# Kernel optimization log

Hardware: AMD Instinct MI355X
Metric: run time of the kernel (lower is better)

The kernel has to match this reference:

```python
import jax, jax.numpy as jnp
import numpy as np

B, S, D = 4, 2048, 1024
H = 16
HD = D // H  # 64


def setup_inputs() -> dict:
    key = jax.random.key(0)
    ks = jax.random.split(key, 8)
    scale = 1.0 / np.sqrt(D)
    return {
        "hidden_states": jax.random.normal(ks[0], (B, S, D), dtype=jnp.float32),
        "attention_mask": jnp.ones((B, 1, 1, S), dtype=jnp.int32),
        "Wq": jax.random.normal(ks[1], (D, D), dtype=jnp.float32) * scale,
        "bq": jax.random.normal(ks[2], (D,), dtype=jnp.float32) * 0.02,
        "Wk": jax.random.normal(ks[3], (D, D), dtype=jnp.float32) * scale,
        "bk": jax.random.normal(ks[4], (D,), dtype=jnp.float32) * 0.02,
        "Wv": jax.random.normal(ks[5], (D, D), dtype=jnp.float32) * scale,
        "bv": jax.random.normal(ks[6], (D,), dtype=jnp.float32) * 0.02,
    }


def _split_heads(x):
    # [b, t, (h d)] -> [b, h, t, d]
    b, t, _ = x.shape
    return x.reshape(b, t, H, HD).transpose(0, 2, 1, 3)


def reference(hidden_states, attention_mask, Wq, bq, Wk, bk, Wv, bv):
    # Linear projections (torch Linear: x @ W.T + b)
    q = _split_heads(hidden_states @ Wq.T + bq)
    k = _split_heads(hidden_states @ Wk.T + bk)
    v = _split_heads(hidden_states @ Wv.T + bv)

    # scaled dot-product scores: [b, h, s, s]
    scores = jnp.einsum("bhqd,bhkd->bhqk", q, k) / np.sqrt(HD)

    s = scores.shape[-1]
    causal = jnp.tril(jnp.ones((s, s), dtype=bool))[None, None]
    neg_inf = jnp.float32(-jnp.inf)
    scores = jnp.where(causal, scores, neg_inf)
    # attention_mask is 0/1 keep mask: [b, 1, 1, s]
    scores = jnp.where(attention_mask == 0, neg_inf, scores)

    probs = jax.nn.softmax(scores, axis=-1)  # dropout p=0 (eval)
    ctx = jnp.einsum("bhqk,bhkd->bhqd", probs, v)
    # [b, h, t, d] -> [b, t, h*d]
    return ctx.transpose(0, 2, 1, 3).reshape(hidden_states.shape[0], s, D)
```

## Files before the change

kernel.cpp:

```cpp
#include <hip/hip_runtime.h>
#include <hip/hip_bf16.h>
#include <math.h>


#define B_ 4
#define S_ 2048
#define D_ 1024
#define H_ 16
#define HD_ 64
#define M_ (B_ * S_)

typedef unsigned short u16;
typedef unsigned int u32;
typedef __attribute__((ext_vector_type(4))) float f32x4;
typedef __attribute__((ext_vector_type(8))) short bf16x8;

__device__ __forceinline__ u16 f2bfu_rn(float x) {
    u32 u = __builtin_bit_cast(u32, x);
    return (u16)((u + 0x8000u) >> 16);
}

__device__ __forceinline__ void gl2lds16(const void* g, void* l) {
    __builtin_amdgcn_global_load_lds(
        (const __attribute__((address_space(1))) u32*)g,
        (__attribute__((address_space(3))) u32*)l, 16, 0, 0);
}

#define XN  8388608u
#define WN  1048576u
__global__ __launch_bounds__(256) void convert_bf16(
    const float* __restrict__ X,  const float* __restrict__ Wq,
    const float* __restrict__ Wk, const float* __restrict__ Wv,
    u16* __restrict__ Xb, u16* __restrict__ Wqb,
    u16* __restrict__ Wkb, u16* __restrict__ Wvb)
{
    size_t idx = ((size_t)blockIdx.x * 256 + threadIdx.x) * 8;
    const float* src; u16* dst; size_t off;
    if (idx < XN)                { src = X;  dst = Xb;  off = idx; }
    else if (idx < XN + WN)      { src = Wq; dst = Wqb; off = idx - XN; }
    else if (idx < XN + 2 * WN)  { src = Wk; dst = Wkb; off = idx - XN - WN; }
    else                         { src = Wv; dst = Wvb; off = idx - XN - 2 * WN; }
    float4 a = *(const float4*)(src + off);
    float4 b = *(const float4*)(src + off + 4);
    uint4 o;
    o.x = (u32)f2bfu_rn(a.x) | ((u32)f2bfu_rn(a.y) << 16);
    o.y = (u32)f2bfu_rn(a.z) | ((u32)f2bfu_rn(a.w) << 16);
    o.z = (u32)f2bfu_rn(b.x) | ((u32)f2bfu_rn(b.y) << 16);
    o.w = (u32)f2bfu_rn(b.z) | ((u32)f2bfu_rn(b.w) << 16);
    *(uint4*)(dst + off) = o;
}

#define QSCALE 0.18033688011112042f

__global__ __launch_bounds__(256) void qkv_mfma(
    const u16* __restrict__ Xb,
    const u16* __restrict__ Wqb, const u16* __restrict__ Wkb,
    const u16* __restrict__ Wvb,
    const float* __restrict__ bq, const float* __restrict__ bk,
    const float* __restrict__ bv,
    u16* __restrict__ Qb, u16* __restrict__ Kb, u16* __restrict__ Vtb)
{
    const int which = blockIdx.z;
    const u16* Asrc; const u16* Bsrc; const float* bias; u16* Out;
    int m0, n0;
    if (which == 0)      { Asrc = Xb;  Bsrc = Wqb; bias = bq; Out = Qb;
                           m0 = blockIdx.y * 128; n0 = blockIdx.x * 128; }
    else if (which == 1) { Asrc = Xb;  Bsrc = Wkb; bias = bk; Out = Kb;
                           m0 = blockIdx.y * 128; n0 = blockIdx.x * 128; }
    else                 { Asrc = Wvb; Bsrc = Xb;  bias = bv; Out = Vtb;
                           m0 = blockIdx.x * 128; n0 = blockIdx.y * 128; }

    __shared__ u16 As[128][64];
    __shared__ u16 Bs[128][64];

    const int t = threadIdx.x;
    const int wave = t >> 6, lane = t & 63;
    const int qd = lane >> 4, l15 = lane & 15;
    const int wm = wave >> 1, wn = wave & 1;

    const f32x4 zero = {0.f, 0.f, 0.f, 0.f};
    f32x4 acc[4][4];
#pragma unroll
    for (int i = 0; i < 4; ++i)
#pragma unroll
        for (int j = 0; j < 4; ++j) acc[i][j] = zero;

    for (int k0 = 0; k0 < D_; k0 += 64) {
        __syncthreads();
#pragma unroll
        for (int i = 0; i < 4; ++i) {
            int r0  = (wave * 4 + i) * 8;
            int row = r0 + (lane >> 3);
            int g   = (lane & 7) ^ (row & 7);
            gl2lds16(Asrc + (size_t)(m0 + row) * D_ + k0 + g * 8, &As[r0][0]);
            gl2lds16(Bsrc + (size_t)(n0 + row) * D_ + k0 + g * 8, &Bs[r0][0]);
        }
        __syncthreads();
#pragma unroll
        for (int ks = 0; ks < 2; ++ks) {
            bf16x8 af[4], bf[4];
#pragma unroll
            for (int mt = 0; mt < 4; ++mt) {
                int row = wm * 64 + mt * 16 + l15;
                int p = (ks * 4 + qd) ^ (row & 7);
                af[mt] = *(const bf16x8*)&As[row][p * 8];
            }
#pragma unroll
            for (int nt = 0; nt < 4; ++nt) {
                int row = wn * 64 + nt * 16 + l15;
                int p = (ks * 4 + qd) ^ (row & 7);
                bf[nt] = *(const bf16x8*)&Bs[row][p * 8];
            }
#pragma unroll
            for (int mt = 0; mt < 4; ++mt)
#pragma unroll
                for (int nt = 0; nt < 4; ++nt)
                    acc[mt][nt] = __builtin_amdgcn_mfma_f32_16x16x32_bf16(
                        af[mt], bf[nt], acc[mt][nt], 0, 0, 0);
        }
    }

    if (which < 2) {
#pragma unroll
        for (int nt = 0; nt < 4; ++nt) {
            int n = n0 + wn * 64 + nt * 16 + l15;
            float bv_ = bias[n];
            int h = n >> 6, hd = n & 63;
#pragma unroll
            for (int mt = 0; mt < 4; ++mt)
#pragma unroll
                for (int r = 0; r < 4; ++r) {
                    int m = m0 + wm * 64 + mt * 16 + qd * 4 + r;
                    int bb = m >> 11, s = m & 2047;
                    float v = acc[mt][nt][r] + bv_;
                    if (which == 0) v *= QSCALE;
                    Out[(((size_t)(bb * H_ + h)) * S_ + s) * HD_ + hd] = f2bfu_rn(v);
                }
        }
    } else {
#pragma unroll
        for (int mt = 0; mt < 4; ++mt)
#pragma unroll
            for (int r = 0; r < 4; ++r) {
                int f = m0 + wm * 64 + mt * 16 + qd * 4 + r;
                float bv_ = bias[f];
                int h = f >> 6, hd = f & 63;
#pragma unroll
                for (int nt = 0; nt < 4; ++nt) {
                    int tok = n0 + wn * 64 + nt * 16 + l15;
                    int bb = tok >> 11, s = tok & 2047;
                    float v = acc[mt][nt][r] + bv_;
                    Out[(((size_t)(bb * H_ + h)) * HD_ + hd) * S_ + s] = f2bfu_rn(v);
                }
            }
    }
}

__global__ __launch_bounds__(256) void attn_chunk(
    const u16* __restrict__ Qb, const u16* __restrict__ Kb,
    const u16* __restrict__ Vtb, const int* __restrict__ amask,
    float* __restrict__ Oout, float* __restrict__ Opart,
    float* __restrict__ L0, float* __restrict__ L1)
{
    const int x = blockIdx.x;
    const int bh = blockIdx.y;
    const int b = bh >> 4, h = bh & 15;

    int qi; bool second;
    if (x < 9)       { qi = 15 - x; second = false; }
    else if (x == 9) { qi = 15;     second = true;  }
    else {
        int p = x - 10, pi = p >> 1;
        second = (p & 1) != 0;
        qi = second ? (14 - pi) : (6 - pi);
    }
    const int q0    = qi * 128;
    const int jtmax = 2 * qi + 1;
    const int jt0   = second ? 16 : 0;
    const int jt1   = second ? jtmax : min(jtmax, 15);

    const int t = threadIdx.x;
    const int wave = t >> 6, lane = t & 63;
    const int qd = lane >> 4, l15 = lane & 15;

    __shared__ u16 Ks[2][64][64];
    __shared__ u16 Vts[2][64][64];
    __shared__ u16 Ps[128][72];
    __shared__ float mb[2][64];

    const size_t base = (size_t)bh * S_ * HD_;
    const u16* Qg = Qb + base;
    const u16* Kg = Kb + base;
    const u16* Vg = Vtb + base;
    const int* am = amask + b * S_;

    bf16x8 qf[2][2];
#pragma unroll
    for (int mt = 0; mt < 2; ++mt) {
        const u16* qrow = Qg + (size_t)(q0 + wave * 32 + mt * 16 + l15) * HD_;
        qf[mt][0] = *(const bf16x8*)(qrow + qd * 8);
        qf[mt][1] = *(const bf16x8*)(qrow + 32 + qd * 8);
    }
    bf16x8 onesf;
    {
        short v = (l15 == 0) ? (short)0x3F80 : (short)0;
        onesf = (bf16x8){v, v, v, v, v, v, v, v};
    }

    const f32x4 zero = {0.f, 0.f, 0.f, 0.f};
    f32x4 o[2][5];
#pragma unroll
    for (int mt = 0; mt < 2; ++mt)
#pragma unroll
        for (int i = 0; i < 5; ++i) o[mt][i] = zero;

    auto STAGE = [&](int jt, int buf) {
        const int j0 = jt * 64;
#pragma unroll
        for (int i = 0; i < 2; ++i) {
            int r0  = (wave * 2 + i) * 8;
            int row = r0 + (lane >> 3);
            int g   = (lane & 7) ^ (row & 7);
            gl2lds16(Kg + (size_t)(j0 + row) * HD_ + g * 8, &Ks[buf][r0][0]);
            gl2lds16(Vg + (size_t)row * S_ + j0 + g * 8, &Vts[buf][r0][0]);
        }
        if (t < 64) mb[buf][t] = (am[j0 + t] == 0) ? -1e30f : 0.0f;
    };

    STAGE(jt0, 0);
    __syncthreads();

    for (int jt = jt0; jt <= jt1; ++jt) {
        const int cb = (jt - jt0) & 1;
        if (jt < jt1) STAGE(jt + 1, cb ^ 1);

        f32x4 sacc[2][4];
#pragma unroll
        for (int mt = 0; mt < 2; ++mt)
#pragma unroll
            for (int nt = 0; nt < 4; ++nt) sacc[mt][nt] = zero;
        __builtin_amdgcn_s_setprio(1);
#pragma unroll
        for (int ks = 0; ks < 2; ++ks) {
#pragma unroll
            for (int nt = 0; nt < 4; ++nt) {
                int brow = nt * 16 + l15;
                int bp = (ks * 4 + qd) ^ (brow & 7);
                bf16x8 bfr = *(const bf16x8*)&Ks[cb][brow][bp * 8];
#pragma unroll
                for (int mt = 0; mt < 2; ++mt)
                    sacc[mt][nt] = __builtin_amdgcn_mfma_f32_16x16x32_bf16(
                        qf[mt][ks], bfr, sacc[mt][nt], 0, 0, 0);
            }
        }
        __builtin_amdgcn_s_setprio(0);

        float bias[4];
#pragma unroll
        for (int nt = 0; nt < 4; ++nt) bias[nt] = mb[cb][nt * 16 + l15];
        const bool nearDiag = (jt >= 2 * qi);
        const int dq = q0 - jt * 64;
#pragma unroll
        for (int mt = 0; mt < 2; ++mt)
#pragma unroll
            for (int r = 0; r < 4; ++r) {
                int prow = wave * 32 + mt * 16 + qd * 4 + r;
#pragma unroll
                for (int nt = 0; nt < 4; ++nt) {
                    int col = nt * 16 + l15;
                    float s = sacc[mt][nt][r] + bias[nt];
                    if (nearDiag && col > prow + dq) s = -1e30f;
                    float p = __builtin_amdgcn_exp2f(s);
                    Ps[prow][col] = f2bfu_rn(p);
                }
            }

        __builtin_amdgcn_s_setprio(1);
#pragma unroll
        for (int ks = 0; ks < 2; ++ks) {
            bf16x8 pf[2];
#pragma unroll
            for (int mt = 0; mt < 2; ++mt)
                pf[mt] = *(const bf16x8*)&Ps[wave * 32 + mt * 16 + l15][ks * 32 + qd * 8];
#pragma unroll
            for (int nt = 0; nt < 4; ++nt) {
                int brow = nt * 16 + l15;
                int bp = (ks * 4 + qd) ^ (brow & 7);
                bf16x8 vf = *(const bf16x8*)&Vts[cb][brow][bp * 8];
#pragma unroll
                for (int mt = 0; mt < 2; ++mt)
                    o[mt][nt] = __builtin_amdgcn_mfma_f32_16x16x32_bf16(
                        pf[mt], vf, o[mt][nt], 0, 0, 0);
            }
#pragma unroll
            for (int mt = 0; mt < 2; ++mt)
                o[mt][4] = __builtin_amdgcn_mfma_f32_16x16x32_bf16(
                    pf[mt], onesf, o[mt][4], 0, 0, 0);
        }
        __builtin_amdgcn_s_setprio(0);

        if (jt < jt1) __syncthreads();
    }

    if (!second) {
        if (qi <= 7) {
#pragma unroll
            for (int mt = 0; mt < 2; ++mt)
#pragma unroll
                for (int r = 0; r < 4; ++r) {
                    float l = __shfl(o[mt][4][r], lane & 48);
                    float inv = 1.0f / l;
                    int q = q0 + wave * 32 + mt * 16 + qd * 4 + r;
                    float* op = Oout + ((size_t)(b * S_ + q)) * D_ + h * HD_;
#pragma unroll
                    for (int nt = 0; nt < 4; ++nt)
                        op[nt * 16 + l15] = o[mt][nt][r] * inv;
                }
        } else {
#pragma unroll
            for (int mt = 0; mt < 2; ++mt)
#pragma unroll
                for (int r = 0; r < 4; ++r) {
                    int q = q0 + wave * 32 + mt * 16 + qd * 4 + r;
                    float* op = Oout + ((size_t)(b * S_ + q)) * D_ + h * HD_;
#pragma unroll
                    for (int nt = 0; nt < 4; ++nt)
                        op[nt * 16 + l15] = o[mt][nt][r];
                    if (l15 == 0) L0[(size_t)bh * S_ + q] = o[mt][4][r];
                }
        }
    } else {
#pragma unroll
        for (int mt = 0; mt < 2; ++mt)
#pragma unroll
            for (int r = 0; r < 4; ++r) {
                int q = q0 + wave * 32 + mt * 16 + qd * 4 + r;
                int sh = q - 1024;
                float* op = Opart + ((size_t)bh * 1024 + sh) * HD_;
#pragma unroll
                for (int nt = 0; nt < 4; ++nt)
                    op[nt * 16 + l15] = o[mt][nt][r];
                if (l15 == 0) L1[(size_t)bh * 1024 + sh] = o[mt][4][r];
            }
    }
}

__global__ __launch_bounds__(256) void combine(
    float* __restrict__ out, const float* __restrict__ Opart,
    const float* __restrict__ L0, const float* __restrict__ L1)
{
    size_t i = ((size_t)blockIdx.x * 256 + threadIdx.x) * 4;
    int d  = (int)(i & (D_ - 1));
    int bs = (int)(i >> 10);
    int b  = bs >> 10, sh = bs & 1023;
    int s  = sh + 1024;
    int h  = d >> 6;
    int bh = b * H_ + h;
    float l = L0[(size_t)bh * S_ + s] + L1[(size_t)bh * 1024 + sh];
    float inv = 1.0f / l;
    float* op = out + ((size_t)(b * S_ + s)) * D_ + d;
    const float* pp = Opart + ((size_t)bh * 1024 + sh) * HD_ + (d & 63);
    float4 v = *(float4*)op;
    float4 p = *(const float4*)pp;
    v.x = (v.x + p.x) * inv; v.y = (v.y + p.y) * inv;
    v.z = (v.z + p.z) * inv; v.w = (v.w + p.w) * inv;
    *(float4*)op = v;
}

extern "C" void kernel_launch(void* const* d_in, const int* in_sizes, int n_in,
                              void* d_out, int out_size, void* d_ws, size_t ws_size,
                              hipStream_t stream) {
    (void)in_sizes; (void)n_in; (void)out_size; (void)ws_size;
    const float* X    = (const float*)d_in[0];
    const int*   mask = (const int*)d_in[1];
    const float* Wq   = (const float*)d_in[2];
    const float* bq   = (const float*)d_in[3];
    const float* Wk   = (const float*)d_in[4];
    const float* bk   = (const float*)d_in[5];
    const float* Wv   = (const float*)d_in[6];
    const float* bv   = (const float*)d_in[7];
    float* out = (float*)d_out;

    u16* Xb  = (u16*)d_ws;
    u16* Wqb = Xb  + XN;
    u16* Wkb = Wqb + WN;
    u16* Wvb = Wkb + WN;
    u16* Qb  = Wvb + WN;
    u16* Kb  = Qb  + XN;
    u16* Vtb = Kb  + XN;
    float* Opart = (float*)(Vtb + XN);
    float* L0 = Opart + (size_t)64 * 1024 * 64;
    float* L1 = L0 + (size_t)64 * 2048;

    convert_bf16<<<(XN + 3 * WN) / (256 * 8), 256, 0, stream>>>(
        X, Wq, Wk, Wv, Xb, Wqb, Wkb, Wvb);
    qkv_mfma<<<dim3(D_ / 128, M_ / 128, 3), 256, 0, stream>>>(
        Xb, Wqb, Wkb, Wvb, bq, bk, bv, Qb, Kb, Vtb);
    attn_chunk<<<dim3(24, B_ * H_), 256, 0, stream>>>(
        Qb, Kb, Vtb, mask, out, Opart, L0, L1);
    combine<<<(B_ * 1024 * D_ / 4) / 256, 256, 0, stream>>>(out, Opart, L0, L1);
}
```

Before: 265.5 us.

## Load K/V fragments directly from global into registers, drop LDS staging

The attention kernel no longer stages K, V^T and mask-bias tiles through double-buffered shared memory with async global-to-LDS loads. Each wave now loads its own K and V MFMA fragments and mask values straight from global memory into registers every tile. This removes the per-tile __syncthreads and the LDS reads. The cost is that each of the wave's loads is redundant across waves and issued without prefetch, so memory latency is exposed and L2 traffic rises.

```diff
diff --git a/kernel.cpp b/kernel.cpp
--- a/kernel.cpp
+++ b/kernel.cpp
@@ -183,10 +183,7 @@
     const int wave = t >> 6, lane = t & 63;
     const int qd = lane >> 4, l15 = lane & 15;
 
-    __shared__ u16 Ks[2][64][64];
-    __shared__ u16 Vts[2][64][64];
     __shared__ u16 Ps[128][72];
-    __shared__ float mb[2][64];
 
     const size_t base = (size_t)bh * S_ * HD_;
     const u16* Qg = Qb + base;
@@ -207,6 +204,9 @@
         onesf = (bf16x8){v, v, v, v, v, v, v, v};
     }
 
+    const u16* kp = Kg + (size_t)l15 * HD_ + qd * 8;
+    const u16* vp = Vg + (size_t)l15 * S_  + qd * 8;
+
     const f32x4 zero = {0.f, 0.f, 0.f, 0.f};
     f32x4 o[2][5];
 #pragma unroll
@@ -214,25 +214,20 @@
 #pragma unroll
         for (int i = 0; i < 5; ++i) o[mt][i] = zero;
 
-    auto STAGE = [&](int jt, int buf) {
+    for (int jt = jt0; jt <= jt1; ++jt) {
         const int j0 = jt * 64;
-#pragma unroll
-        for (int i = 0; i < 2; ++i) {
-            int r0  = (wave * 2 + i) * 8;
-            int row = r0 + (lane >> 3);
-            int g   = (lane & 7) ^ (row & 7);
-            gl2lds16(Kg + (size_t)(j0 + row) * HD_ + g * 8, &Ks[buf][r0][0]);
-            gl2lds16(Vg + (size_t)row * S_ + j0 + g * 8, &Vts[buf][r0][0]);
-        }
-        if (t < 64) mb[buf][t] = (am[j0 + t] == 0) ? -1e30f : 0.0f;
-    };
-
-    STAGE(jt0, 0);
-    __syncthreads();
-
-    for (int jt = jt0; jt <= jt1; ++jt) {
-        const int cb = (jt - jt0) & 1;
-        if (jt < jt1) STAGE(jt + 1, cb ^ 1);
+
+        bf16x8 kf[2][4];
+#pragma unroll
+        for (int ks = 0; ks < 2; ++ks)
+#pragma unroll
+            for (int nt = 0; nt < 4; ++nt)
+                kf[ks][nt] = *(const bf16x8*)(kp + (size_t)(j0 + nt * 16) * HD_ + ks * 32);
+
+        float bias[4];
+#pragma unroll
+        for (int nt = 0; nt < 4; ++nt)
+            bias[nt] = (am[j0 + nt * 16 + l15] == 0) ? -1e30f : 0.0f;
 
         f32x4 sacc[2][4];
 #pragma unroll
@@ -241,25 +236,24 @@
             for (int nt = 0; nt < 4; ++nt) sacc[mt][nt] = zero;
         __builtin_amdgcn_s_setprio(1);
 #pragma unroll
-        for (int ks = 0; ks < 2; ++ks) {
-#pragma unroll
-            for (int nt = 0; nt < 4; ++nt) {
-                int brow = nt * 16 + l15;
-                int bp = (ks * 4 + qd) ^ (brow & 7);
-                bf16x8 bfr = *(const bf16x8*)&Ks[cb][brow][bp * 8];
+        for (int ks = 0; ks < 2; ++ks)
+#pragma unroll
+            for (int nt = 0; nt < 4; ++nt)
 #pragma unroll
                 for (int mt = 0; mt < 2; ++mt)
                     sacc[mt][nt] = __builtin_amdgcn_mfma_f32_16x16x32_bf16(
-                        qf[mt][ks], bfr, sacc[mt][nt], 0, 0, 0);
-            }
-        }
+                        qf[mt][ks], kf[ks][nt], sacc[mt][nt], 0, 0, 0);
         __builtin_amdgcn_s_setprio(0);
 
-        float bias[4];
-#pragma unroll
-        for (int nt = 0; nt < 4; ++nt) bias[nt] = mb[cb][nt * 16 + l15];
+        bf16x8 vf[2][4];
+#pragma unroll
+        for (int ks = 0; ks < 2; ++ks)
+#pragma unroll
+            for (int nt = 0; nt < 4; ++nt)
+                vf[ks][nt] = *(const bf16x8*)(vp + (size_t)(nt * 16) * S_ + j0 + ks * 32);
+
         const bool nearDiag = (jt >= 2 * qi);
-        const int dq = q0 - jt * 64;
+        const int dq = q0 - j0;
 #pragma unroll
         for (int mt = 0; mt < 2; ++mt)
 #pragma unroll
@@ -283,23 +277,17 @@
             for (int mt = 0; mt < 2; ++mt)
                 pf[mt] = *(const bf16x8*)&Ps[wave * 32 + mt * 16 + l15][ks * 32 + qd * 8];
 #pragma unroll
-            for (int nt = 0; nt < 4; ++nt) {
-                int brow = nt * 16 + l15;
-                int bp = (ks * 4 + qd) ^ (brow & 7);
-                bf16x8 vf = *(const bf16x8*)&Vts[cb][brow][bp * 8];
+            for (int nt = 0; nt < 4; ++nt)
 #pragma unroll
                 for (int mt = 0; mt < 2; ++mt)
                     o[mt][nt] = __builtin_amdgcn_mfma_f32_16x16x32_bf16(
-                        pf[mt], vf, o[mt][nt], 0, 0, 0);
-            }
+                        pf[mt], vf[ks][nt], o[mt][nt], 0, 0, 0);
 #pragma unroll
             for (int mt = 0; mt < 2; ++mt)
                 o[mt][4] = __builtin_amdgcn_mfma_f32_16x16x32_bf16(
                     pf[mt], onesf, o[mt][4], 0, 0, 0);
         }
         __builtin_amdgcn_s_setprio(0);
-
-        if (jt < jt1) __syncthreads();
     }
 
     if (!second) {
```

New measurement: 352.5 us. 32.8% more time.
